# Optimization experiments

Measured on AMD Instinct MI355X. Metric: run time of the kernel, lower is better.

The kernel has to match this reference:

```python
import jax, jax.numpy as jnp
import numpy as np

B, S, K = 2, 1024, 8          # batch, seq_len (multiple of 128), f2p fan-out
D, H, DH = 256, 8, 32          # d_model, heads, head_dim
FF = 1024                      # ffn hidden
DC, DT = 384, 384              # col-name / text value embedding dims
NB = 2                         # relational blocks
NEG = -1e9


def _ln(x, g, b):
    m = x.mean(-1, keepdims=True)
    v = ((x - m) ** 2).mean(-1, keepdims=True)
    return (x - m) / jnp.sqrt(v + 1e-5) * g + b


def _mha(h, wq, wk, wv, wo, mask):
    # h: (B,S,D); mask: (B,S,S) bool
    b, s, _ = h.shape
    q = (h @ wq).reshape(b, s, H, DH)
    k = (h @ wk).reshape(b, s, H, DH)
    v = (h @ wv).reshape(b, s, H, DH)
    scores = jnp.einsum('bqhd,bkhd->bhqk', q, k) / np.float32(np.sqrt(DH))
    scores = jnp.where(mask[:, None], scores, NEG)
    p = jax.nn.softmax(scores, axis=-1)
    # fully-masked rows output zero (flex-attention semantics)
    p = p * mask.any(-1)[:, None, :, None]
    o = jnp.einsum('bhqk,bkhd->bqhd', p, v).reshape(b, s, D)
    return o @ wo


def setup_inputs() -> dict:
    key = jax.random.key(0)
    ks = list(jax.random.split(key, 64))
    it = iter(ks)
    nk = lambda: next(it)
    sc = lambda *shape: jax.random.normal(nk(), shape, dtype=jnp.float32) * 0.02
    inp = {}
    inp['node_idxs'] = jax.random.randint(nk(), (B, S), 0, 256)
    inp['f2p_nbr_idxs'] = jax.random.randint(nk(), (B, S, K), 0, 256)
    inp['col_name_idxs'] = jax.random.randint(nk(), (B, S), 0, 64)
    inp['table_name_idxs'] = jax.random.randint(nk(), (B, S), 0, 8)
    inp['is_padding'] = jnp.zeros((B, S), dtype=bool)
    inp['sem_types'] = jax.random.randint(nk(), (B, S), 0, 2)
    inp['masks'] = jax.random.randint(nk(), (B, S), 0, 2).astype(bool)
    inp['col_name_values'] = jax.random.normal(nk(), (B, S, DC), dtype=jnp.float32)
    inp['number_values'] = jax.random.normal(nk(), (B, S, 1), dtype=jnp.float32)
    inp['text_values'] = jax.random.normal(nk(), (B, S, DT), dtype=jnp.float32)
    # cell-value encoders + per-type layernorms
    inp['W_col'] = sc(DC, D); inp['b_col'] = jnp.zeros(D)
    inp['W_num'] = sc(1, D);  inp['b_num'] = jnp.zeros(D)
    inp['W_text'] = sc(DT, D); inp['b_text'] = jnp.zeros(D)
    for t in ('col', 'num', 'text'):
        inp['g_' + t] = jnp.ones(D); inp['be_' + t] = jnp.zeros(D)
    inp['me_num'] = sc(D); inp['me_text'] = sc(D)
    # relational blocks: 4 masked attentions (feat/nbr/col/full) per block
    inp['Wq'] = sc(NB, 4, D, D); inp['Wk'] = sc(NB, 4, D, D)
    inp['Wv'] = sc(NB, 4, D, D); inp['Wo'] = sc(NB, 4, D, D)
    inp['ln1_g'] = jnp.ones((NB, D)); inp['ln1_b'] = jnp.zeros((NB, D))
    inp['ln2_g'] = jnp.ones((NB, D)); inp['ln2_b'] = jnp.zeros((NB, D))
    inp['W1'] = sc(NB, D, FF); inp['b1'] = jnp.zeros((NB, FF))
    inp['W2'] = sc(NB, FF, D); inp['b2'] = jnp.zeros((NB, D))
    inp['g_out'] = jnp.ones(D); inp['be_out'] = jnp.zeros(D)
    return inp


def reference(node_idxs, f2p_nbr_idxs, col_name_idxs, table_name_idxs,
              is_padding, sem_types, masks,
              col_name_values, number_values, text_values,
              W_col, b_col, W_num, b_num, W_text, b_text,
              g_col, be_col, g_num, be_num, g_text, be_text,
              me_num, me_text,
              Wq, Wk, Wv, Wo, ln1_g, ln1_b, ln2_g, ln2_b,
              W1, b1, W2, b2, g_out, be_out):
    notpad = ~is_padding
    # --- pairwise mask construction (the kernel-headroom hot spot) ---
    pad = notpad[:, :, None] & notpad[:, None, :]                     # (B,S,S)
    same_node = node_idxs[:, :, None] == node_idxs[:, None, :]
    kv_in_f2p = (node_idxs[:, None, :, None] == f2p_nbr_idxs[:, :, None, :]).any(-1)
    q_in_f2p = (node_idxs[:, :, None, None] == f2p_nbr_idxs[:, None, :, :]).any(-1)
    same_col_table = (col_name_idxs[:, :, None] == col_name_idxs[:, None, :]) & \
                     (table_name_idxs[:, :, None] == table_name_idxs[:, None, :])
    attn_masks = [(same_node | kv_in_f2p) & pad,   # feat
                  q_in_f2p & pad,                  # nbr
                  same_col_table & pad,            # col
                  pad]                             # full
    # --- cell value encoding ---
    x = _ln(col_name_values @ W_col + b_col, g_col, be_col) * notpad[..., None]
    sel_num = (sem_types == 0) & notpad
    x = x + _ln(number_values @ W_num + b_num, g_num, be_num) * (sel_num & ~masks)[..., None]
    x = x + me_num * (sel_num & masks)[..., None]
    sel_text = (sem_types == 1) & notpad
    x = x + _ln(text_values @ W_text + b_text, g_text, be_text) * (sel_text & ~masks)[..., None]
    x = x + me_text * (sel_text & masks)[..., None]
    # --- relational blocks ---
    for i in range(NB):
        h = _ln(x, ln1_g[i], ln1_b[i])
        a = jnp.zeros_like(x)
        for l in range(4):
            a = a + _mha(h, Wq[i, l], Wk[i, l], Wv[i, l], Wo[i, l], attn_masks[l])
        x = x + a
        h2 = _ln(x, ln2_g[i], ln2_b[i])
        x = x + jax.nn.gelu(h2 @ W1[i] + b1[i]) @ W2[i] + b2[i]
    return _ln(x, g_out, be_out)
```

## Files before the change

### kernel.cpp

```cpp
#include <hip/hip_runtime.h>
#include <stdint.h>

#define TOKS 2048
#define SEQ 1024

typedef __attribute__((ext_vector_type(8))) short short8;
typedef __attribute__((ext_vector_type(4))) float f32x4;

__device__ __forceinline__ float loadf(const void* p, size_t i, int isbf16) {
  if (isbf16) {
    unsigned short u = ((const unsigned short*)p)[i];
    return __uint_as_float(((unsigned)u) << 16);
  }
  return ((const float*)p)[i];
}
__device__ __forceinline__ unsigned short f32_to_bf16(float f) {
  unsigned u = __float_as_uint(f);
  unsigned r = u + 0x7FFFu + ((u >> 16) & 1u);
  return (unsigned short)(r >> 16);
}
__device__ __forceinline__ float bf2f(unsigned short u) {
  return __uint_as_float(((unsigned)u) << 16);
}
__device__ __forceinline__ unsigned cvtpk(float a, float b) {
  unsigned r;
  asm("v_cvt_pk_bf16_f32 %0, %1, %2" : "=v"(r) : "v"(a), "v"(b));
  return r;
}
__device__ __forceinline__ unsigned short cvt1(float a) {
  return (unsigned short)cvtpk(a, a);
}
__device__ __forceinline__ int readbool(const void* p, size_t i, int isb) {
  return isb ? (((const unsigned char*)p)[i] != 0) : (((const int*)p)[i] != 0);
}

__global__ void k_detect(const void* fs, const void* bs, int* flags) {
  int lane = threadIdx.x;
  int bad = 0;
  for (int i = lane; i < 256; i += 64) {
    unsigned short u = ((const unsigned short*)fs)[i];
    float v = __uint_as_float(((unsigned)u) << 16);
    if (!(fabsf(v) <= 100.f)) bad = 1;
  }
  int big = 0;
  for (int i = lane; i < 512; i += 64) {
    if (((const unsigned*)bs)[i] > 1u) big = 1;
  }
#pragma unroll
  for (int off = 32; off; off >>= 1) {
    bad |= __shfl_xor(bad, off);
    big |= __shfl_xor(big, off);
  }
  if (lane == 0) { flags[0] = bad ? 0 : 1; flags[1] = big ? 1 : 0; }
}

struct ConvEntry { const void* src; void* dst; int n; int mode; };
struct TEntry { const void* src; unsigned short* dst; int soff, K, N, pitch; };
struct PrepArgs {
  ConvEntry ce[23];
  TEntry te[38];
  const int* node; const int* f2p; const int* colid; const int* tabid;
  const void* pad; unsigned short* W4m;
};

__global__ __launch_bounds__(256) void k_prep(PrepArgs pa, const int* __restrict__ flags) {
  __shared__ float t[32][33];
  __shared__ int kn[64], kcl[64], ktb[64], kpd[64], kf2[64][8];
  int y = blockIdx.y;
  int tid = threadIdx.x;
  int isbf = flags[0];

  if (y < 23) {
    ConvEntry E = pa.ce[y];
    if (E.mode == 0) {
      float* d = (float*)E.dst;
      for (int i = blockIdx.x * 256 + tid; i < E.n; i += gridDim.x * 256)
        d[i] = loadf(E.src, (size_t)i, isbf);
    } else {
      unsigned short* d = (unsigned short*)E.dst;
      for (int i = blockIdx.x * 256 + tid; i < E.n; i += gridDim.x * 256)
        d[i] = f32_to_bf16(loadf(E.src, (size_t)i, isbf));
    }
    return;
  }
  if (y < 61) {
    TEntry E = pa.te[y - 23];
    int ktiles = E.K >> 5, ntiles = E.N >> 5;
    if ((int)blockIdx.x >= ktiles * ntiles) return;
    int tk = blockIdx.x % ktiles, tn = blockIdx.x / ktiles;
    int tx = tid & 31, ty = tid >> 5;
#pragma unroll
    for (int s = 0; s < 4; s++) {
      int k = tk * 32 + ty + s * 8, n = tn * 32 + tx;
      t[ty + s * 8][tx] = loadf(E.src, (size_t)E.soff + (size_t)k * E.N + n, isbf);
    }
    __syncthreads();
#pragma unroll
    for (int s = 0; s < 4; s++) {
      int n = tn * 32 + ty + s * 8, k = tk * 32 + tx;
      E.dst[(size_t)n * E.pitch + k] = f32_to_bf16(t[tx][ty + s * 8]);
    }
    return;
  }

  int z = y - 61;
  int b = z >> 2, l = z & 3;
  int base = b * SEQ;
  int kc = blockIdx.x & 15, qbg = blockIdx.x >> 4;
  int isb = flags[1];
  if (tid < 64) {
    int kkey = base + kc * 64 + tid;
    kn[tid] = pa.node[kkey];
    kcl[tid] = pa.colid[kkey];
    ktb[tid] = pa.tabid[kkey];
    kpd[tid] = readbool(pa.pad, kkey, isb) ? 0 : 1;
    if (l == 1) {
#pragma unroll
      for (int j = 0; j < 8; j++) kf2[tid][j] = pa.f2p[(size_t)kkey * 8 + j];
    }
  }
  __syncthreads();

  int wave = tid >> 6, lane = tid & 63;
  int qb = qbg * 4 + wave;
  int q = lane & 15;
  int qq = base + qb * 16 + q;
  int qn_l = pa.node[qq];
  int qpd_l = readbool(pa.pad, qq, isb) ? 0 : 1;
  int qcl_l = 0, qtb_l = 0, qf2_l[8];
  if (l == 2) { qcl_l = pa.colid[qq]; qtb_l = pa.tabid[qq]; }
  if (l == 0) {
#pragma unroll
    for (int j = 0; j < 8; j++) qf2_l[j] = pa.f2p[(size_t)qq * 8 + j];
  }

  unsigned w = 0;
#pragma unroll
  for (int t4 = 0; t4 < 4; t4++) {
#pragma unroll
    for (int r = 0; r < 4; r++) {
      int kl = t4 * 16 + (lane >> 4) * 4 + r;
      int sel;
      if (l == 0) {
        int nk = kn[kl];
        sel = (qn_l == nk);
#pragma unroll
        for (int j = 0; j < 8; j++) sel |= (qf2_l[j] == nk);
      } else if (l == 1) {
        sel = (qn_l == kf2[kl][0]) | (qn_l == kf2[kl][1]) | (qn_l == kf2[kl][2]) |
              (qn_l == kf2[kl][3]) | (qn_l == kf2[kl][4]) | (qn_l == kf2[kl][5]) |
              (qn_l == kf2[kl][6]) | (qn_l == kf2[kl][7]);
      } else if (l == 2) {
        sel = (qcl_l == kcl[kl]) & (qtb_l == ktb[kl]);
      } else {
        sel = 1;
      }
      w |= (unsigned)(sel & qpd_l & kpd[kl]) << (4 * t4 + r);
    }
  }
  pa.W4m[((size_t)((z * 32 + (qb >> 1)) * 2 + (qb & 1)) << 10) + kc * 64 + lane] =
      (unsigned short)w;
}

__device__ __forceinline__ float block_sum256(float v, float* red) {
#pragma unroll
  for (int off = 32; off; off >>= 1) v += __shfl_xor(v, off);
  int w = threadIdx.x >> 6;
  __syncthreads();
  if ((threadIdx.x & 63) == 0) red[w] = v;
  __syncthreads();
  return red[0] + red[1] + red[2] + red[3];
}
__device__ __forceinline__ float ln256(float y, float* red) {
  float mean = block_sum256(y, red) * (1.0f / 256.0f);
  float dv = y - mean;
  float var = block_sum256(dv * dv, red) * (1.0f / 256.0f);
  return dv * rsqrtf(var + 1e-5f);
}

__global__ __launch_bounds__(256) void k_encoder3(
    const float* __restrict__ Yc, const float* __restrict__ Yt,
    const float* __restrict__ numv,
    const float* __restrict__ Wn, const float* __restrict__ bn,
    const float* __restrict__ gc, const float* __restrict__ bec,
    const float* __restrict__ gn, const float* __restrict__ ben,
    const float* __restrict__ gt, const float* __restrict__ bet,
    const float* __restrict__ men, const float* __restrict__ met,
    const void* __restrict__ pad_raw, const void* __restrict__ msk_raw,
    const int* __restrict__ flags, const int* __restrict__ sem,
    const float* __restrict__ l1g, const float* __restrict__ l1b,
    float* __restrict__ x, unsigned short* __restrict__ h) {
  __shared__ float red[4];
  int token = blockIdx.x, d = threadIdx.x;
  int isb = flags[1];
  int ispad = readbool(pad_raw, token, isb);
  float notpad = ispad ? 0.f : 1.f;
  int st = sem[token];
  int mk = readbool(msk_raw, token, isb);

  float yc = Yc[(size_t)token * 256 + d];
  float xv = (ln256(yc, red) * gc[d] + bec[d]) * notpad;

  {
    float yn = numv[token] * Wn[d] + bn[d];
    float lnv = ln256(yn, red) * gn[d] + ben[d];
    if (st == 0 && !ispad && !mk) xv += lnv;
    if (st == 0 && !ispad && mk)  xv += men[d];
  }
  if (st == 1 && !ispad && !mk) {
    float yt = Yt[(size_t)token * 256 + d];
    xv += ln256(yt, red) * gt[d] + bet[d];
  }
  if (st == 1 && !ispad && mk) xv += met[d];
  x[(size_t)token * 256 + d] = xv;
  h[(size_t)token * 256 + d] = f32_to_bf16(ln256(xv, red) * l1g[d] + l1b[d]);
}

__global__ __launch_bounds__(256) void k_ln_add_bf4(
    float* __restrict__ x, const float* __restrict__ p0, const float* __restrict__ p1,
    const float* __restrict__ g, const float* __restrict__ b,
    unsigned short* __restrict__ out) {
  int wave = threadIdx.x >> 6, lane = threadIdx.x & 63;
  int token = blockIdx.x * 4 + wave;
  size_t base = (size_t)token * 256 + lane * 4;
  float4 xv = *(const float4*)&x[base];
  float4 a = *(const float4*)&p0[base];
  float4 c = *(const float4*)&p1[base];
  xv.x += a.x + c.x; xv.y += a.y + c.y; xv.z += a.z + c.z; xv.w += a.w + c.w;
  *(float4*)&x[base] = xv;
  float s = (xv.x + xv.y) + (xv.z + xv.w);
#pragma unroll
  for (int off = 1; off < 64; off <<= 1) s += __shfl_xor(s, off);
  float mean = s * 0.00390625f;
  float4 dv = {xv.x - mean, xv.y - mean, xv.z - mean, xv.w - mean};
  float vs = (dv.x * dv.x + dv.y * dv.y) + (dv.z * dv.z + dv.w * dv.w);
#pragma unroll
  for (int off = 1; off < 64; off <<= 1) vs += __shfl_xor(vs, off);
  float rstd = rsqrtf(vs * 0.00390625f + 1e-5f);
  float4 gg = *(const float4*)&g[lane * 4];
  float4 bb = *(const float4*)&b[lane * 4];
  float o0 = dv.x * rstd * gg.x + bb.x;
  float o1 = dv.y * rstd * gg.y + bb.y;
  float o2 = dv.z * rstd * gg.z + bb.z;
  float o3 = dv.w * rstd * gg.w + bb.w;
  uint2 o;
  o.x = cvtpk(o0, o1);
  o.y = cvtpk(o2, o3);
  *(uint2*)&out[base] = o;
}

__global__ __launch_bounds__(256) void k_ln_out_add4(
    const float* __restrict__ xin, const float* __restrict__ p0,
    const float* __restrict__ p1, const float* __restrict__ g,
    const float* __restrict__ b, void* __restrict__ out,
    const int* __restrict__ flags) {
  int wave = threadIdx.x >> 6, lane = threadIdx.x & 63;
  int token = blockIdx.x * 4 + wave;
  size_t base = (size_t)token * 256 + lane * 4;
  float4 xv = *(const float4*)&xin[base];
  float4 a = *(const float4*)&p0[base];
  float4 c = *(const float4*)&p1[base];
  xv.x += a.x + c.x; xv.y += a.y + c.y; xv.z += a.z + c.z; xv.w += a.w + c.w;
  float s = (xv.x + xv.y) + (xv.z + xv.w);
#pragma unroll
  for (int off = 1; off < 64; off <<= 1) s += __shfl_xor(s, off);
  float mean = s * 0.00390625f;
  float4 dv = {xv.x - mean, xv.y - mean, xv.z - mean, xv.w - mean};
  float vs = (dv.x * dv.x + dv.y * dv.y) + (dv.z * dv.z + dv.w * dv.w);
#pragma unroll
  for (int off = 1; off < 64; off <<= 1) vs += __shfl_xor(vs, off);
  float rstd = rsqrtf(vs * 0.00390625f + 1e-5f);
  float4 gg = *(const float4*)&g[lane * 4];
  float4 bb = *(const float4*)&b[lane * 4];
  float o0 = dv.x * rstd * gg.x + bb.x;
  float o1 = dv.y * rstd * gg.y + bb.y;
  float o2 = dv.z * rstd * gg.z + bb.z;
  float o3 = dv.w * rstd * gg.w + bb.w;
  if (flags[0]) {
    uint2 o;
    o.x = cvtpk(o0, o1);
    o.y = cvtpk(o2, o3);
    *(uint2*)&((unsigned short*)out)[base] = o;
  } else {
    float4 o = {o0, o1, o2, o3};
    *(float4*)&((float*)out)[base] = o;
  }
}

__device__ __forceinline__ float gelu_tanh(float v) {
  const float c = 0.7978845608028654f;
  float t = tanhf(c * (v + 0.044715f * v * v * v));
  return 0.5f * v * (1.f + t);
}

template <int BM, int BN, int ACT, int OUT, int KS>
__global__ __launch_bounds__(256) void k_gemm_bf(
    const unsigned short* __restrict__ A, const unsigned short* __restrict__ Bt,
    const float* __restrict__ bias, void* __restrict__ Cv,
    unsigned short* __restrict__ Qhp, unsigned short* __restrict__ Khp,
    unsigned short* __restrict__ VTp,
    int M, int N, int K) {
  if (OUT == 3 && blockIdx.z) {
    A += 786432;
    Bt += 98304;
    bias += 256;
    Cv = (void*)((float*)Cv + 524288);
  }
  __shared__ __align__(16) unsigned short As[BM][40];
  __shared__ __align__(16) unsigned short Bs[BN][40];
  constexpr int FI = BM / 32, FJ = BN / 32;
  int tid = threadIdx.x, wave = tid >> 6, lane = tid & 63;
  int g = lane >> 4, c = lane & 15;
  int wr = wave >> 1, wc = wave & 1;
  int bm = blockIdx.y * BM, bn = blockIdx.x * BN;
  int kz = (KS > 1) ? blockIdx.z : 0;
  f32x4 acc[FI][FJ] = {};
  int sr = tid >> 2, ss = (tid & 3) * 8;
  int kbeg = kz * (K / KS), kend = kbeg + K / KS;

  for (int k0 = kbeg; k0 < kend; k0 += 32) {
    __syncthreads();
#pragma unroll
    for (int rr = 0; rr < BM; rr += 64)
      *(short8*)&As[rr + sr][ss] = *(const short8*)&A[(size_t)(bm + rr + sr) * K + k0 + ss];
#pragma unroll
    for (int rr = 0; rr < BN; rr += 64)
      *(short8*)&Bs[rr + sr][ss] = *(const short8*)&Bt[(size_t)(bn + rr + sr) * K + k0 + ss];
    __syncthreads();
    short8 af[FI], bf[FJ];
#pragma unroll
    for (int i = 0; i < FI; i++) af[i] = *(short8*)&As[wr * (BM / 2) + i * 16 + c][g * 8];
#pragma unroll
    for (int j = 0; j < FJ; j++) bf[j] = *(short8*)&Bs[wc * (BN / 2) + j * 16 + c][g * 8];
#pragma unroll
    for (int i = 0; i < FI; i++)
#pragma unroll
      for (int j = 0; j < FJ; j++)
        acc[i][j] = __builtin_amdgcn_mfma_f32_16x16x32_bf16(af[i], bf[j], acc[i][j], 0, 0, 0);
  }

#pragma unroll
  for (int i = 0; i < FI; i++)
#pragma unroll
    for (int j = 0; j < FJ; j++) {
      int col = bn + wc * (BN / 2) + j * 16 + c;
      int row0 = bm + wr * (BM / 2) + i * 16 + g * 4;
      if (OUT == 2) {
        int ll = col / 768, cm = col - ll * 768;
        int w = cm >> 8;
        int hh = (cm & 255) >> 5, dd = cm & 31;
        int hd = ((row0 >> 10) * 4 + ll) * 8 + hh;
        int tok = row0 & 1023;
        if (w == 2) {
          uint2 pk;
          pk.x = cvtpk(acc[i][j][0], acc[i][j][1]);
          pk.y = cvtpk(acc[i][j][2], acc[i][j][3]);
          *(uint2*)&VTp[(size_t)(hd * 32 + dd) * 1024 + tok] = pk;
        } else {
          unsigned short* dst = (w == 0 ? Qhp : Khp) + (size_t)hd * 32768 + tok * 32 + dd;
          float scl = (w == 0) ? 0.25503487f : 1.f;
#pragma unroll
          for (int r = 0; r < 4; r++) dst[r * 32] = cvt1(acc[i][j][r] * scl);
        }
      } else {
#pragma unroll
        for (int r = 0; r < 4; r++) {
          float v = acc[i][j][r];
          if (bias && kz == 0) v += bias[col];
          if (ACT) v = gelu_tanh(v);
          size_t idx = (size_t)(row0 + r) * N + col;
          if (OUT == 1) ((unsigned short*)Cv)[idx] = cvt1(v);
          else ((float*)Cv)[(size_t)kz * M * N + idx] = v;
        }
      }
    }
}

__global__ __launch_bounds__(256) void k_attn6(
    const unsigned short* __restrict__ Qh, const unsigned short* __restrict__ Kh,
    const unsigned short* __restrict__ W4m, const unsigned short* __restrict__ VT,
    unsigned short* __restrict__ Ocat) {
  __shared__ __align__(16) unsigned short Pl[4][64][72];
  __shared__ float lsv[4][64];
  int bid = blockIdx.x;
  int z = bid & 7, h = (bid >> 3) & 7, qi = bid >> 6;
  int b = z >> 2, l = z & 3;
  int tid = threadIdx.x;
  int wave = tid >> 6, lane = tid & 63;
  int g = lane >> 4, c = lane & 15;
  int q0 = qi * 64;
  size_t tokbase = (size_t)b * SEQ;
  int hd = z * 8 + h;
  size_t hbase = (size_t)hd * 32768;
  const unsigned short* vbase = VT + hbase;
  const unsigned short* mbase = W4m + (((size_t)(z * 64 + qi * 4)) << 10) + lane;

  short8 qf[4];
#pragma unroll
  for (int s = 0; s < 4; s++)
    qf[s] = *(const short8*)&Qh[hbase + (size_t)(q0 + s * 16 + c) * 32 + g * 8];

  f32x4 zero = {0.f, 0.f, 0.f, 0.f};
  f32x4 oacc[4][2];
#pragma unroll
  for (int s = 0; s < 4; s++) { oacc[s][0] = zero; oacc[s][1] = zero; }
  float ls[4] = {0.f, 0.f, 0.f, 0.f};

#pragma unroll
  for (int ci = 0; ci < 4; ci++) {
    int kc = wave * 4 + ci;
    int kb0 = kc * 64;
    short8 kf[4];
#pragma unroll
    for (int t = 0; t < 4; t++)
      kf[t] = *(const short8*)&Kh[hbase + (size_t)(kb0 + t * 16 + c) * 32 + g * 8];
    unsigned mw[4];
#pragma unroll
    for (int s = 0; s < 4; s++)
      mw[s] = mbase[(size_t)s * 1024 + kc * 64];

#pragma unroll
    for (int s = 0; s < 4; s++) {
      f32x4 sa[4];
      __builtin_amdgcn_s_setprio(1);
#pragma unroll
      for (int t = 0; t < 4; t++)
        sa[t] = __builtin_amdgcn_mfma_f32_16x16x32_bf16(kf[t], qf[s], zero, 0, 0, 0);
      __builtin_amdgcn_s_setprio(0);
#pragma unroll
      for (int t = 0; t < 4; t++) {
        float pv[4];
#pragma unroll
        for (int r = 0; r < 4; r++) {
          float p = __builtin_amdgcn_exp2f(sa[t][r]);
          int ok = (mw[s] >> (4 * t + r)) & 1;
          pv[r] = ok ? p : 0.f;
        }
        ls[s] += (pv[0] + pv[1]) + (pv[2] + pv[3]);
        uint2 w2;
        w2.x = cvtpk(pv[0], pv[1]);
        w2.y = cvtpk(pv[2], pv[3]);
        *(uint2*)&Pl[wave][s * 16 + c][t * 16 + g * 4] = w2;
      }
    }

#pragma unroll
    for (int k2 = 0; k2 < 2; k2++) {
      short8 v0 = *(const short8*)&vbase[(size_t)c * 1024 + kb0 + k2 * 32 + g * 8];
      short8 v1 = *(const short8*)&vbase[(size_t)(c + 16) * 1024 + kb0 + k2 * 32 + g * 8];
      __builtin_amdgcn_s_setprio(1);
#pragma unroll
      for (int s = 0; s < 4; s++) {
        short8 pa = *(short8*)&Pl[wave][s * 16 + c][k2 * 32 + g * 8];
        oacc[s][0] = __builtin_amdgcn_mfma_f32_16x16x32_bf16(pa, v0, oacc[s][0], 0, 0, 0);
        oacc[s][1] = __builtin_amdgcn_mfma_f32_16x16x32_bf16(pa, v1, oacc[s][1], 0, 0, 0);
      }
      __builtin_amdgcn_s_setprio(0);
    }
  }

#pragma unroll
  for (int s = 0; s < 4; s++) {
    ls[s] += __shfl_xor(ls[s], 16);
    ls[s] += __shfl_xor(ls[s], 32);
  }
  {
    float* ob = (float*)&Pl[wave][0][0];
#pragma unroll
    for (int s = 0; s < 4; s++) {
      if (g == 0) lsv[wave][s * 16 + c] = ls[s];
#pragma unroll
      for (int r = 0; r < 4; r++) {
        ob[(s * 16 + g * 4 + r) * 33 + c] = oacc[s][0][r];
        ob[(s * 16 + g * 4 + r) * 33 + 16 + c] = oacc[s][1][r];
      }
    }
  }
  __syncthreads();
  {
#pragma unroll
    for (int r = 0; r < 4; r++) {
      int row = wave * 16 + g * 4 + r;
      float lst = 0.f, o0 = 0.f, o1 = 0.f;
#pragma unroll
      for (int j = 0; j < 4; j++) {
        lst += lsv[j][row];
        const float* ob = (const float*)&Pl[j][0][0];
        o0 += ob[row * 33 + c];
        o1 += ob[row * 33 + 16 + c];
      }
      float inv = (lst > 0.f) ? (1.f / lst) : 0.f;
      size_t grow = tokbase + q0 + row;
      unsigned short* op = &Ocat[grow * 1024 + l * 256 + h * 32];
      op[c] = cvt1(o0 * inv);
      op[c + 16] = cvt1(o1 * inv);
    }
  }
}

extern "C" void kernel_launch(void* const* d_in, const int* in_sizes, int n_in,
                              void* d_out, int out_size, void* d_ws, size_t ws_size,
                              hipStream_t stream) {
  (void)n_in; (void)out_size; (void)ws_size;
  char* wsb = (char*)d_ws;
  int* flags = (int*)wsb;
  float* fbase = (float*)(wsb + 256);
  size_t fo = 0;
  auto alloc = [&](size_t n) { float* p = fbase + fo; fo += (n + 63) & ~(size_t)63; return p; };

  float* bc = alloc(512);    float* bt = bc + 256;
  float* Wn = alloc(256);    float* bn = alloc(256);
  float* gc = alloc(256);    float* bec = alloc(256);
  float* gn = alloc(256);    float* ben = alloc(256);
  float* gt = alloc(256);    float* bet = alloc(256);
  float* men = alloc(256);   float* met = alloc(256);
  float* l1g = alloc(512);   float* l1b = alloc(512);
  float* l2g = alloc(512);   float* l2b = alloc(512);
  float* b1c = alloc(2048);  float* b2c = alloc(512);
  float* goc = alloc(256);   float* beo = alloc(256);
  float* numv = alloc(2048);
  float* x = alloc(524288);
  unsigned short* W4m   = (unsigned short*)alloc(262144);
  unsigned short* h     = (unsigned short*)alloc(262144);
  unsigned short* WqkvT = (unsigned short*)alloc(786432);
  unsigned short* WoT   = (unsigned short*)alloc(262144);
  unsigned short* W1T   = (unsigned short*)alloc(262144);
  unsigned short* W2T   = (unsigned short*)alloc(262144);
  unsigned short* WcT   = (unsigned short*)alloc(98304);
  unsigned short* WtT   = WcT + 98304;
  unsigned short* colvb = (unsigned short*)alloc(786432);
  unsigned short* textvb= colvb + 786432;
  unsigned short* fbuf  = (unsigned short*)alloc(1048576);
  unsigned short* Ocat  = (unsigned short*)alloc(1048576);
  unsigned short* Qh    = (unsigned short*)alloc(1048576);
  unsigned short* Kh    = (unsigned short*)alloc(1048576);
  float* VTf            = alloc(1048576);
  unsigned short* VT    = (unsigned short*)VTf;
  float* p0 = VTf;
  float* p1 = VTf + 524288;

  k_detect<<<1, 64, 0, stream>>>(d_in[7], d_in[6], flags);

  PrepArgs pa;
  const int idxs[21] = {11, 12, 13, 15, 16, 17, 18, 19, 20, 21, 22, 23,
                        28, 29, 30, 31, 33, 35, 36, 37, 8};
  float* dsts[21] = {bc, Wn, bn, bt, gc, bec, gn, ben, gt, bet, men, met,
                     l1g, l1b, l2g, l2b, b1c, b2c, goc, beo, numv};
  for (int t = 0; t < 21; t++) {
    pa.ce[t].src = d_in[idxs[t]];
    pa.ce[t].dst = dsts[t];
    pa.ce[t].n = in_sizes[idxs[t]];
    pa.ce[t].mode = 0;
  }
  pa.ce[21].src = d_in[7]; pa.ce[21].dst = colvb;  pa.ce[21].n = 786432; pa.ce[21].mode = 1;
  pa.ce[22].src = d_in[9]; pa.ce[22].dst = textvb; pa.ce[22].n = 786432; pa.ce[22].mode = 1;

  int ne = 0;
  for (int i = 0; i < 2; i++)
    for (int l = 0; l < 4; l++)
      for (int w = 0; w < 3; w++) {
        pa.te[ne].src = d_in[24 + w];
        pa.te[ne].soff = (i * 4 + l) * 65536;
        pa.te[ne].dst = WqkvT + (size_t)i * 786432 + (size_t)(l * 768 + w * 256) * 256;
        pa.te[ne].K = 256; pa.te[ne].N = 256; pa.te[ne].pitch = 256;
        ne++;
      }
  for (int i = 0; i < 2; i++)
    for (int l = 0; l < 4; l++) {
      pa.te[ne].src = d_in[27];
      pa.te[ne].soff = (i * 4 + l) * 65536;
      pa.te[ne].dst = WoT + (size_t)i * 262144 + l * 256;
      pa.te[ne].K = 256; pa.te[ne].N = 256; pa.te[ne].pitch = 1024;
      ne++;
    }
  for (int i = 0; i < 2; i++) {
    pa.te[ne].src = d_in[32];
    pa.te[ne].soff = i * 262144;
    pa.te[ne].dst = W1T + (size_t)i * 262144;
    pa.te[ne].K = 256; pa.te[ne].N = 1024; pa.te[ne].pitch = 256;
    ne++;
  }
  for (int i = 0; i < 2; i++) {
    pa.te[ne].src = d_in[34];
    pa.te[ne].soff = i * 262144;
    pa.te[ne].dst = W2T + (size_t)i * 262144;
    pa.te[ne].K = 1024; pa.te[ne].N = 256; pa.te[ne].pitch = 1024;
    ne++;
  }
  pa.te[ne].src = d_in[10]; pa.te[ne].soff = 0; pa.te[ne].dst = WcT;
  pa.te[ne].K = 384; pa.te[ne].N = 256; pa.te[ne].pitch = 384; ne++;
  pa.te[ne].src = d_in[14]; pa.te[ne].soff = 0; pa.te[ne].dst = WtT;
  pa.te[ne].K = 384; pa.te[ne].N = 256; pa.te[ne].pitch = 384; ne++;

  pa.node = (const int*)d_in[0]; pa.f2p = (const int*)d_in[1];
  pa.colid = (const int*)d_in[2]; pa.tabid = (const int*)d_in[3];
  pa.pad = d_in[4]; pa.W4m = W4m;

  k_prep<<<dim3(256, 69), 256, 0, stream>>>(pa, flags);

  k_gemm_bf<128, 128, 0, 3, 1><<<dim3(2, 16, 2), 256, 0, stream>>>(
      colvb, WcT, bc, p0, nullptr, nullptr, nullptr, 2048, 256, 384);
  k_encoder3<<<2048, 256, 0, stream>>>(p0, p1, numv, Wn, bn, gc, bec, gn, ben,
                                       gt, bet, men, met, d_in[4], d_in[6], flags,
                                       (const int*)d_in[5], l1g, l1b, x, h);

  for (int i = 0; i < 2; i++) {
    k_gemm_bf<128, 128, 0, 2, 1><<<dim3(24, 16), 256, 0, stream>>>(
        h, WqkvT + (size_t)i * 786432, nullptr, nullptr, Qh, Kh, VT, 2048, 3072, 256);
    k_attn6<<<1024, 256, 0, stream>>>(Qh, Kh, W4m, VT, Ocat);
    k_gemm_bf<64, 64, 0, 0, 2><<<dim3(4, 32, 2), 256, 0, stream>>>(
        Ocat, WoT + (size_t)i * 262144, nullptr, p0, nullptr, nullptr, nullptr, 2048, 256, 1024);
    k_ln_add_bf4<<<512, 256, 0, stream>>>(x, p0, p1, l2g + i * 256, l2b + i * 256, h);
    k_gemm_bf<128, 64, 1, 1, 1><<<dim3(16, 16), 256, 0, stream>>>(
        h, W1T + (size_t)i * 262144, b1c + (size_t)i * 1024, fbuf, nullptr, nullptr, nullptr,
        2048, 1024, 256);
    k_gemm_bf<64, 64, 0, 0, 2><<<dim3(4, 32, 2), 256, 0, stream>>>(
        fbuf, W2T + (size_t)i * 262144, b2c + (size_t)i * 256, p0, nullptr, nullptr, nullptr,
        2048, 256, 1024);
    if (i == 0)
      k_ln_add_bf4<<<512, 256, 0, stream>>>(x, p0, p1, l1g + 256, l1b + 256, h);
    else
      k_ln_out_add4<<<512, 256, 0, stream>>>(x, p0, p1, goc, beo, d_out, flags);
  }
}
```

Before: 214.2 us.

## Double attention query tile per block and fold dtype detection into consumers

The attention kernel now processes 128 query rows per block instead of 64, halving the grid and reusing each loaded K/V tile across twice as many queries, with LDS moved to dynamic shared memory sized for the larger tile. The separate single-wave detection launch is removed, and each consumer kernel recomputes the bf16 and bool-width flags inline from the inputs. This trades one fewer launch and less K/V traffic for higher register and LDS pressure in attention, fewer blocks (512) to fill the GPU, and redundant detection loads in every block.

```diff
diff --git a/kernel.cpp b/kernel.cpp
--- a/kernel.cpp
+++ b/kernel.cpp
@@ -19,9 +19,6 @@
   unsigned r = u + 0x7FFFu + ((u >> 16) & 1u);
   return (unsigned short)(r >> 16);
 }
-__device__ __forceinline__ float bf2f(unsigned short u) {
-  return __uint_as_float(((unsigned)u) << 16);
-}
 __device__ __forceinline__ unsigned cvtpk(float a, float b) {
   unsigned r;
   asm("v_cvt_pk_bf16_f32 %0, %1, %2" : "=v"(r) : "v"(a), "v"(b));
@@ -33,25 +30,22 @@
 __device__ __forceinline__ int readbool(const void* p, size_t i, int isb) {
   return isb ? (((const unsigned char*)p)[i] != 0) : (((const int*)p)[i] != 0);
 }
-
-__global__ void k_detect(const void* fs, const void* bs, int* flags) {
-  int lane = threadIdx.x;
+__device__ __forceinline__ void detect2(const void* fs, const void* bs,
+                                        int& isbf, int& isb) {
+  int lane = threadIdx.x & 63;
   int bad = 0;
-  for (int i = lane; i < 256; i += 64) {
-    unsigned short u = ((const unsigned short*)fs)[i];
+#pragma unroll
+  for (int s = 0; s < 4; s++) {
+    unsigned short u = ((const unsigned short*)fs)[lane * 4 + s];
     float v = __uint_as_float(((unsigned)u) << 16);
-    if (!(fabsf(v) <= 100.f)) bad = 1;
+    bad |= !(fabsf(v) <= 100.f);
   }
   int big = 0;
-  for (int i = lane; i < 512; i += 64) {
-    if (((const unsigned*)bs)[i] > 1u) big = 1;
-  }
-#pragma unroll
-  for (int off = 32; off; off >>= 1) {
-    bad |= __shfl_xor(bad, off);
-    big |= __shfl_xor(big, off);
-  }
-  if (lane == 0) { flags[0] = bad ? 0 : 1; flags[1] = big ? 1 : 0; }
+#pragma unroll
+  for (int s = 0; s < 8; s++)
+    big |= (((const unsigned*)bs)[lane * 8 + s] > 1u);
+  isbf = __any(bad) ? 0 : 1;
+  isb = __any(big) ? 1 : 0;
 }
 
 struct ConvEntry { const void* src; void* dst; int n; int mode; };
@@ -61,14 +55,16 @@
   TEntry te[38];
   const int* node; const int* f2p; const int* colid; const int* tabid;
   const void* pad; unsigned short* W4m;
+  const void* fs; const void* bs;
 };
 
-__global__ __launch_bounds__(256) void k_prep(PrepArgs pa, const int* __restrict__ flags) {
+__global__ __launch_bounds__(256) void k_prep(PrepArgs pa) {
   __shared__ float t[32][33];
   __shared__ int kn[64], kcl[64], ktb[64], kpd[64], kf2[64][8];
   int y = blockIdx.y;
   int tid = threadIdx.x;
-  int isbf = flags[0];
+  int isbf, isb;
+  detect2(pa.fs, pa.bs, isbf, isb);
 
   if (y < 23) {
     ConvEntry E = pa.ce[y];
@@ -107,7 +103,6 @@
   int b = z >> 2, l = z & 3;
   int base = b * SEQ;
   int kc = blockIdx.x & 15, qbg = blockIdx.x >> 4;
-  int isb = flags[1];
   if (tid < 64) {
     int kkey = base + kc * 64 + tid;
     kn[tid] = pa.node[kkey];
@@ -187,12 +182,14 @@
     const float* __restrict__ gt, const float* __restrict__ bet,
     const float* __restrict__ men, const float* __restrict__ met,
     const void* __restrict__ pad_raw, const void* __restrict__ msk_raw,
-    const int* __restrict__ flags, const int* __restrict__ sem,
+    const void* __restrict__ fs, const void* __restrict__ bs,
+    const int* __restrict__ sem,
     const float* __restrict__ l1g, const float* __restrict__ l1b,
     float* __restrict__ x, unsigned short* __restrict__ h) {
   __shared__ float red[4];
   int token = blockIdx.x, d = threadIdx.x;
-  int isb = flags[1];
+  int isbf, isb;
+  detect2(fs, bs, isbf, isb);
   int ispad = readbool(pad_raw, token, isb);
   float notpad = ispad ? 0.f : 1.f;
   int st = sem[token];
@@ -253,9 +250,12 @@
     const float* __restrict__ xin, const float* __restrict__ p0,
     const float* __restrict__ p1, const float* __restrict__ g,
     const float* __restrict__ b, void* __restrict__ out,
-    const int* __restrict__ flags) {
+    const void* __restrict__ fs, const void* __restrict__ bs) {
   int wave = threadIdx.x >> 6, lane = threadIdx.x & 63;
   int token = blockIdx.x * 4 + wave;
+  int isbf, isb;
+  detect2(fs, bs, isbf, isb);
+  (void)isb;
   size_t base = (size_t)token * 256 + lane * 4;
   float4 xv = *(const float4*)&xin[base];
   float4 a = *(const float4*)&p0[base];
@@ -276,7 +276,7 @@
   float o1 = dv.y * rstd * gg.y + bb.y;
   float o2 = dv.z * rstd * gg.z + bb.z;
   float o3 = dv.w * rstd * gg.w + bb.w;
-  if (flags[0]) {
+  if (isbf) {
     uint2 o;
     o.x = cvtpk(o0, o1);
     o.y = cvtpk(o2, o3);
@@ -376,35 +376,37 @@
     }
 }
 
-__global__ __launch_bounds__(256) void k_attn6(
+__global__ __launch_bounds__(256) void k_attn7(
     const unsigned short* __restrict__ Qh, const unsigned short* __restrict__ Kh,
     const unsigned short* __restrict__ W4m, const unsigned short* __restrict__ VT,
     unsigned short* __restrict__ Ocat) {
-  __shared__ __align__(16) unsigned short Pl[4][64][72];
-  __shared__ float lsv[4][64];
+  extern __shared__ char smem[];
+  unsigned short* Pl = (unsigned short*)smem;
+  float* lsv = (float*)(smem + 4 * 128 * 72 * 2);
   int bid = blockIdx.x;
   int z = bid & 7, h = (bid >> 3) & 7, qi = bid >> 6;
   int b = z >> 2, l = z & 3;
   int tid = threadIdx.x;
   int wave = tid >> 6, lane = tid & 63;
   int g = lane >> 4, c = lane & 15;
-  int q0 = qi * 64;
+  int q0 = qi * 128;
   size_t tokbase = (size_t)b * SEQ;
   int hd = z * 8 + h;
   size_t hbase = (size_t)hd * 32768;
   const unsigned short* vbase = VT + hbase;
-  const unsigned short* mbase = W4m + (((size_t)(z * 64 + qi * 4)) << 10) + lane;
-
-  short8 qf[4];
-#pragma unroll
-  for (int s = 0; s < 4; s++)
+  const unsigned short* mbase = W4m + (((size_t)(z * 64 + qi * 8)) << 10) + lane;
+  unsigned short* Pw = Pl + (size_t)wave * 128 * 72;
+
+  short8 qf[8];
+#pragma unroll
+  for (int s = 0; s < 8; s++)
     qf[s] = *(const short8*)&Qh[hbase + (size_t)(q0 + s * 16 + c) * 32 + g * 8];
 
   f32x4 zero = {0.f, 0.f, 0.f, 0.f};
-  f32x4 oacc[4][2];
-#pragma unroll
-  for (int s = 0; s < 4; s++) { oacc[s][0] = zero; oacc[s][1] = zero; }
-  float ls[4] = {0.f, 0.f, 0.f, 0.f};
+  f32x4 oacc[8][2];
+#pragma unroll
+  for (int s = 0; s < 8; s++) { oacc[s][0] = zero; oacc[s][1] = zero; }
+  float ls[8] = {};
 
 #pragma unroll
   for (int ci = 0; ci < 4; ci++) {
@@ -414,13 +416,13 @@
 #pragma unroll
     for (int t = 0; t < 4; t++)
       kf[t] = *(const short8*)&Kh[hbase + (size_t)(kb0 + t * 16 + c) * 32 + g * 8];
-    unsigned mw[4];
-#pragma unroll
-    for (int s = 0; s < 4; s++)
+    unsigned mw[8];
+#pragma unroll
+    for (int s = 0; s < 8; s++)
       mw[s] = mbase[(size_t)s * 1024 + kc * 64];
 
 #pragma unroll
-    for (int s = 0; s < 4; s++) {
+    for (int s = 0; s < 8; s++) {
       f32x4 sa[4];
       __builtin_amdgcn_s_setprio(1);
 #pragma unroll
@@ -440,7 +442,7 @@
         uint2 w2;
         w2.x = cvtpk(pv[0], pv[1]);
         w2.y = cvtpk(pv[2], pv[3]);
-        *(uint2*)&Pl[wave][s * 16 + c][t * 16 + g * 4] = w2;
+        *(uint2*)&Pw[(size_t)(s * 16 + c) * 72 + t * 16 + g * 4] = w2;
       }
     }
 
@@ -450,8 +452,8 @@
       short8 v1 = *(const short8*)&vbase[(size_t)(c + 16) * 1024 + kb0 + k2 * 32 + g * 8];
       __builtin_amdgcn_s_setprio(1);
 #pragma unroll
-      for (int s = 0; s < 4; s++) {
-        short8 pa = *(short8*)&Pl[wave][s * 16 + c][k2 * 32 + g * 8];
+      for (int s = 0; s < 8; s++) {
+        short8 pa = *(short8*)&Pw[(size_t)(s * 16 + c) * 72 + k2 * 32 + g * 8];
         oacc[s][0] = __builtin_amdgcn_mfma_f32_16x16x32_bf16(pa, v0, oacc[s][0], 0, 0, 0);
         oacc[s][1] = __builtin_amdgcn_mfma_f32_16x16x32_bf16(pa, v1, oacc[s][1], 0, 0, 0);
       }
@@ -460,15 +462,15 @@
   }
 
 #pragma unroll
-  for (int s = 0; s < 4; s++) {
+  for (int s = 0; s < 8; s++) {
     ls[s] += __shfl_xor(ls[s], 16);
     ls[s] += __shfl_xor(ls[s], 32);
   }
   {
-    float* ob = (float*)&Pl[wave][0][0];
-#pragma unroll
-    for (int s = 0; s < 4; s++) {
-      if (g == 0) lsv[wave][s * 16 + c] = ls[s];
+    float* ob = (float*)Pw;
+#pragma unroll
+    for (int s = 0; s < 8; s++) {
+      if (g == 0) lsv[wave * 128 + s * 16 + c] = ls[s];
 #pragma unroll
       for (int r = 0; r < 4; r++) {
         ob[(s * 16 + g * 4 + r) * 33 + c] = oacc[s][0][r];
@@ -479,13 +481,13 @@
   __syncthreads();
   {
 #pragma unroll
-    for (int r = 0; r < 4; r++) {
-      int row = wave * 16 + g * 4 + r;
+    for (int rr = 0; rr < 8; rr++) {
+      int row = wave * 32 + g * 8 + rr;
       float lst = 0.f, o0 = 0.f, o1 = 0.f;
 #pragma unroll
       for (int j = 0; j < 4; j++) {
-        lst += lsv[j][row];
-        const float* ob = (const float*)&Pl[j][0][0];
+        lst += lsv[j * 128 + row];
+        const float* ob = (const float*)(Pl + (size_t)j * 128 * 72);
         o0 += ob[row * 33 + c];
         o1 += ob[row * 33 + 16 + c];
       }
@@ -503,7 +505,6 @@
                               hipStream_t stream) {
   (void)n_in; (void)out_size; (void)ws_size;
   char* wsb = (char*)d_ws;
-  int* flags = (int*)wsb;
   float* fbase = (float*)(wsb + 256);
   size_t fo = 0;
   auto alloc = [&](size_t n) { float* p = fbase + fo; fo += (n + 63) & ~(size_t)63; return p; };
@@ -539,8 +540,6 @@
   float* p0 = VTf;
   float* p1 = VTf + 524288;
 
-  k_detect<<<1, 64, 0, stream>>>(d_in[7], d_in[6], flags);
-
   PrepArgs pa;
   const int idxs[21] = {11, 12, 13, 15, 16, 17, 18, 19, 20, 21, 22, 23,
                         28, 29, 30, 31, 33, 35, 36, 37, 8};
@@ -595,19 +594,22 @@
   pa.node = (const int*)d_in[0]; pa.f2p = (const int*)d_in[1];
   pa.colid = (const int*)d_in[2]; pa.tabid = (const int*)d_in[3];
   pa.pad = d_in[4]; pa.W4m = W4m;
-
-  k_prep<<<dim3(256, 69), 256, 0, stream>>>(pa, flags);
+  pa.fs = d_in[7]; pa.bs = d_in[6];
+
+  k_prep<<<dim3(256, 69), 256, 0, stream>>>(pa);
 
   k_gemm_bf<128, 128, 0, 3, 1><<<dim3(2, 16, 2), 256, 0, stream>>>(
       colvb, WcT, bc, p0, nullptr, nullptr, nullptr, 2048, 256, 384);
   k_encoder3<<<2048, 256, 0, stream>>>(p0, p1, numv, Wn, bn, gc, bec, gn, ben,
-                                       gt, bet, men, met, d_in[4], d_in[6], flags,
+                                       gt, bet, men, met, d_in[4], d_in[6],
+                                       d_in[7], d_in[6],
                                        (const int*)d_in[5], l1g, l1b, x, h);
 
+  const int attn_lds = 4 * 128 * 72 * 2 + 4 * 128 * 4;
   for (int i = 0; i < 2; i++) {
     k_gemm_bf<128, 128, 0, 2, 1><<<dim3(24, 16), 256, 0, stream>>>(
         h, WqkvT + (size_t)i * 786432, nullptr, nullptr, Qh, Kh, VT, 2048, 3072, 256);
-    k_attn6<<<1024, 256, 0, stream>>>(Qh, Kh, W4m, VT, Ocat);
+    k_attn7<<<512, 256, attn_lds, stream>>>(Qh, Kh, W4m, VT, Ocat);
     k_gemm_bf<64, 64, 0, 0, 2><<<dim3(4, 32, 2), 256, 0, stream>>>(
         Ocat, WoT + (size_t)i * 262144, nullptr, p0, nullptr, nullptr, nullptr, 2048, 256, 1024);
     k_ln_add_bf4<<<512, 256, 0, stream>>>(x, p0, p1, l2g + i * 256, l2b + i * 256, h);
@@ -620,6 +622,7 @@
     if (i == 0)
       k_ln_add_bf4<<<512, 256, 0, stream>>>(x, p0, p1, l1g + 256, l1b + 256, h);
     else
-      k_ln_out_add4<<<512, 256, 0, stream>>>(x, p0, p1, goc, beo, d_out, flags);
-  }
-}
+      k_ln_out_add4<<<512, 256, 0, stream>>>(x, p0, p1, goc, beo, d_out,
+                                             d_in[7], d_in[6]);
+  }
+}
```

Measured after the change: 213.4 us. About the same (-0.4%).
